# Optimization experiments

Measured on AMD Instinct MI355X. Metric: run time of the kernel, lower is better.

## Reference

```python
import jax, jax.numpy as jnp
import numpy as np

N_NODES = 50000
N_EDGES = 800000
N_FEAT = 128
HIDDEN = 64
N_CLASSES = 16


def setup_inputs() -> dict:
    key = jax.random.key(0)
    ks = jax.random.split(key, 8)
    x = jax.random.normal(ks[0], (N_NODES, N_FEAT), dtype=jnp.float32)
    edge_index = jax.random.randint(ks[1], (2, N_EDGES), 0, N_NODES, dtype=jnp.int64)
    # GCNConv weights (glorot-like) and biases
    W1 = jax.random.normal(ks[2], (N_FEAT, HIDDEN), dtype=jnp.float32) / np.sqrt(N_FEAT)
    b1 = jnp.zeros((HIDDEN,), dtype=jnp.float32)
    W2 = jax.random.normal(ks[3], (HIDDEN, HIDDEN), dtype=jnp.float32) / np.sqrt(HIDDEN)
    b2 = jnp.zeros((HIDDEN,), dtype=jnp.float32)
    Wout = jax.random.normal(ks[4], (HIDDEN, N_CLASSES), dtype=jnp.float32) / np.sqrt(HIDDEN)
    bout = jnp.zeros((N_CLASSES,), dtype=jnp.float32)
    return {"x": x, "edge_index": edge_index, "W1": W1, "b1": b1,
            "W2": W2, "b2": b2, "Wout": Wout, "bout": bout}


def _gcn_conv(h, src, dst, norm, W, b, n_nodes):
    # h: [N, F_in]; linear transform then normalized scatter-add aggregation
    h = h @ W                                   # [N, F_out]
    msg = h[src] * norm[:, None]                # gather + scale  [E+N, F_out]
    out = jax.ops.segment_sum(msg, dst, num_segments=n_nodes)  # scatter-add
    return out + b


def reference(x, edge_index, W1, b1, W2, b2, Wout, bout):
    n = x.shape[0]
    # add self-loops (PyG GCNConv default add_self_loops=True)
    loops = jnp.arange(n, dtype=edge_index.dtype)
    src = jnp.concatenate([edge_index[0], loops])
    dst = jnp.concatenate([edge_index[1], loops])
    # symmetric normalization: deg^-1/2[src] * deg^-1/2[dst] (edge_weight = 1)
    ones = jnp.ones(src.shape[0], dtype=x.dtype)
    deg = jax.ops.segment_sum(ones, dst, num_segments=n)
    dinv = jnp.where(deg > 0, jax.lax.rsqrt(jnp.maximum(deg, 1e-12)), 0.0)
    norm = dinv[src] * dinv[dst]

    h = _gcn_conv(x, src, dst, norm, W1, b1, n)
    h = jax.nn.relu(h)
    # dropout p=0.5 with training=False -> identity
    h = _gcn_conv(h, src, dst, norm, W2, b2, n)
    h = jax.nn.relu(h)
    logits = h @ Wout + bout
    return jax.nn.softmax(logits, axis=1)
```

## Files before the change

kernel.cpp:

```cpp
#include <hip/hip_runtime.h>
#include <hip/hip_fp16.h>

#define N_NODES 50000
#define N_EDGES 800000
#define N_FEAT 128
#define HIDDEN 64
#define N_CLASSES 16
#define NBLK_NODE 196
#define TCAP 8192

typedef _Float16 f16x8 __attribute__((ext_vector_type(8)));
typedef float f32x4 __attribute__((ext_vector_type(4)));

__global__ void k_init(int* __restrict__ tileCur) {
    int tid = threadIdx.x;
    if (tid < NBLK_NODE) tileCur[tid] = tid * TCAP;
}

__global__ __launch_bounds__(256) void k_part(const int* __restrict__ ei,
                                              int* __restrict__ tileCur,
                                              int* __restrict__ binned) {
    __shared__ int cnt[NBLK_NODE], base[NBLK_NODE], cur[NBLK_NODE];
    int tid = threadIdx.x;
    int start = blockIdx.x * 4096;
    if (tid < NBLK_NODE) cnt[tid] = 0;
    __syncthreads();
    int s[16], d[16];
#pragma unroll
    for (int u = 0; u < 4; ++u) {
        int e0 = start + u * 1024 + tid * 4;
        if (e0 + 4 <= N_EDGES) {
            int4 s4 = *(const int4*)&ei[e0];
            int4 d4 = *(const int4*)&ei[N_EDGES + e0];
            s[u * 4 + 0] = s4.x; s[u * 4 + 1] = s4.y; s[u * 4 + 2] = s4.z; s[u * 4 + 3] = s4.w;
            d[u * 4 + 0] = d4.x; d[u * 4 + 1] = d4.y; d[u * 4 + 2] = d4.z; d[u * 4 + 3] = d4.w;
#pragma unroll
            for (int q = 0; q < 4; ++q) atomicAdd(&cnt[d[u * 4 + q] >> 8], 1);
        } else {
#pragma unroll
            for (int q = 0; q < 4; ++q) {
                int e = e0 + q;
                if (e < N_EDGES) {
                    s[u * 4 + q] = ei[e];
                    d[u * 4 + q] = ei[N_EDGES + e];
                    atomicAdd(&cnt[d[u * 4 + q] >> 8], 1);
                } else s[u * 4 + q] = -1;
            }
        }
    }
    __syncthreads();
    if (tid < NBLK_NODE) {
        base[tid] = atomicAdd(&tileCur[tid], cnt[tid]);
        cur[tid] = 0;
    }
    __syncthreads();
#pragma unroll
    for (int u = 0; u < 16; ++u) {
        if (s[u] < 0) continue;
        int t = d[u] >> 8;
        int r = atomicAdd(&cur[t], 1);
        int p = base[t] + r;
        if (p < (t + 1) * TCAP)
            binned[p] = s[u] | ((d[u] & 255) << 16);
    }
}

__global__ __launch_bounds__(256) void k_finesort(const int* __restrict__ binned,
                                                  const int* __restrict__ tileCur,
                                                  int* __restrict__ csr,
                                                  int2* __restrict__ rse,
                                                  float* __restrict__ dinv) {
    __shared__ int stage[TCAP];
    __shared__ int sc[256];
    __shared__ int cnt256[256];
    __shared__ int nodeOff[256];
    int tid = threadIdx.x;
    int tb = blockIdx.x;
    int beg = tb * TCAP;
    int m = tileCur[tb] - beg;
    if (m > TCAP) m = TCAP;
    cnt256[tid] = 0;
    __syncthreads();
    const int4* b4 = (const int4*)(binned + beg);
    int nv = m >> 2;
    for (int i = tid; i < nv; i += 256) {
        int4 r = b4[i];
        atomicAdd(&cnt256[(r.x >> 16) & 255], 1);
        atomicAdd(&cnt256[(r.y >> 16) & 255], 1);
        atomicAdd(&cnt256[(r.z >> 16) & 255], 1);
        atomicAdd(&cnt256[(r.w >> 16) & 255], 1);
    }
    for (int i = (m & ~3) + tid; i < m; i += 256)
        atomicAdd(&cnt256[(binned[beg + i] >> 16) & 255], 1);
    __syncthreads();
    int myc = cnt256[tid];
    sc[tid] = myc;
    __syncthreads();
#pragma unroll
    for (int off = 1; off < 256; off <<= 1) {
        int t = (tid >= off) ? sc[tid - off] : 0;
        __syncthreads();
        sc[tid] += t;
        __syncthreads();
    }
    int off0 = sc[tid] - myc;
    nodeOff[tid] = off0;
    int gnode = tb * 256 + tid;
    if (gnode < N_NODES) {
        dinv[gnode] = rsqrtf((float)myc + 1.0f);
        rse[gnode] = make_int2(beg + off0, myc);
    }
    cnt256[tid] = 0;
    __syncthreads();
    for (int i = tid; i < nv; i += 256) {
        int4 r = b4[i];
        int rr;
        rr = atomicAdd(&cnt256[(r.x >> 16) & 255], 1); stage[nodeOff[(r.x >> 16) & 255] + rr] = r.x & 0xFFFF;
        rr = atomicAdd(&cnt256[(r.y >> 16) & 255], 1); stage[nodeOff[(r.y >> 16) & 255] + rr] = r.y & 0xFFFF;
        rr = atomicAdd(&cnt256[(r.z >> 16) & 255], 1); stage[nodeOff[(r.z >> 16) & 255] + rr] = r.z & 0xFFFF;
        rr = atomicAdd(&cnt256[(r.w >> 16) & 255], 1); stage[nodeOff[(r.w >> 16) & 255] + rr] = r.w & 0xFFFF;
    }
    for (int i = (m & ~3) + tid; i < m; i += 256) {
        int rec = binned[beg + i];
        int dl = (rec >> 16) & 255;
        int rr = atomicAdd(&cnt256[dl], 1);
        stage[nodeOff[dl] + rr] = rec & 0xFFFF;
    }
    __syncthreads();
    int4* c4 = (int4*)(csr + beg);
    for (int i = tid; i < nv; i += 256) c4[i] = ((const int4*)stage)[i];
    for (int i = (m & ~3) + tid; i < m; i += 256) csr[beg + i] = stage[i];
}

template <int K, typename TIn>
__global__ __launch_bounds__(256) void k_mm(const TIn* __restrict__ a,
                                            const float* __restrict__ w,
                                            const float* __restrict__ dinv,
                                            __half* __restrict__ out) {
    constexpr int LDK = K + 8;
    __shared__ __align__(16) __half A_lds[64 * LDK];
    __shared__ __align__(16) __half Wt_lds[64 * LDK];
    int tid = threadIdx.x;
    long nbase = (long)blockIdx.x * 64;

    for (int i = tid; i < K * 16; i += 256) {
        int k = (i * 4) >> 6;
        int f0 = (i * 4) & 63;
        float4 v = *(const float4*)&w[i * 4];
        Wt_lds[(f0 + 0) * LDK + k] = __float2half(v.x);
        Wt_lds[(f0 + 1) * LDK + k] = __float2half(v.y);
        Wt_lds[(f0 + 2) * LDK + k] = __float2half(v.z);
        Wt_lds[(f0 + 3) * LDK + k] = __float2half(v.w);
    }
    for (int i = tid; i < 64 * K / 8; i += 256) {
        int n = (i * 8) / K;
        int k0 = (i * 8) % K;
        long gn = nbase + n;
        if constexpr (sizeof(TIn) == 4) {
            float4 v0, v1;
            if (gn < N_NODES) {
                v0 = *(const float4*)&a[gn * K + k0];
                v1 = *(const float4*)&a[gn * K + k0 + 4];
            } else {
                v0 = make_float4(0.f, 0.f, 0.f, 0.f);
                v1 = v0;
            }
            __half2* dst = (__half2*)&A_lds[n * LDK + k0];
            dst[0] = __floats2half2_rn(v0.x, v0.y);
            dst[1] = __floats2half2_rn(v0.z, v0.w);
            dst[2] = __floats2half2_rn(v1.x, v1.y);
            dst[3] = __floats2half2_rn(v1.z, v1.w);
        } else {
            int4 v = (gn < N_NODES) ? *(const int4*)&a[gn * K + k0]
                                    : make_int4(0, 0, 0, 0);
            *(int4*)&A_lds[n * LDK + k0] = v;
        }
    }
    __syncthreads();

    int wv = tid >> 6;
    int lane = tid & 63;
    int m = lane & 15;
    int quad = lane >> 4;
    const __half* Arow = &A_lds[(wv * 16 + m) * LDK + quad * 8];
    f32x4 acc[4] = {};
#pragma unroll
    for (int t = 0; t < K; t += 32) {
        f16x8 af = *(const f16x8*)(const void*)&Arow[t];
#pragma unroll
        for (int g = 0; g < 4; ++g) {
            f16x8 bf = *(const f16x8*)(const void*)&Wt_lds[(g * 16 + m) * LDK + t + quad * 8];
            acc[g] = __builtin_amdgcn_mfma_f32_16x16x32_f16(af, bf, acc[g], 0, 0, 0);
        }
    }

#pragma unroll
    for (int r = 0; r < 4; ++r) {
        int n = wv * 16 + quad * 4 + r;
        long gn = nbase + n;
        if (gn < N_NODES) {
            float di = dinv[gn];
#pragma unroll
            for (int g = 0; g < 4; ++g)
                out[gn * HIDDEN + g * 16 + m] = __float2half(acc[g][r] * di);
        }
    }
}

__device__ __forceinline__ void acc_row8(float* a, int4 rv) {
    float2 f;
    f = __half22float2(*(__half2*)&rv.x); a[0] += f.x; a[1] += f.y;
    f = __half22float2(*(__half2*)&rv.y); a[2] += f.x; a[3] += f.y;
    f = __half22float2(*(__half2*)&rv.z); a[4] += f.x; a[5] += f.y;
    f = __half22float2(*(__half2*)&rv.w); a[6] += f.x; a[7] += f.y;
}

__global__ void k_gather(const __half* __restrict__ h, const int* __restrict__ csr,
                         const int2* __restrict__ rse, const float* __restrict__ dinv,
                         const float* __restrict__ bias, __half* __restrict__ out) {
    int t = blockIdx.x * 256 + threadIdx.x;
    int node = __builtin_amdgcn_readfirstlane(t >> 6);
    int lane = t & 63;
    int e8 = lane >> 3;
    int q = lane & 7;
    int2 se = rse[node];
    int r0 = se.x, r1 = se.x + se.y;
    float dd = dinv[node];

    float a[8] = {0.f, 0.f, 0.f, 0.f, 0.f, 0.f, 0.f, 0.f};
    if (e8 == 0)
        acc_row8(a, *(const int4*)&h[(long)node * HIDDEN + q * 8]);

    int j = r0;
    while (j + 16 <= r1) {
        int sA = csr[j + e8];
        int sB = csr[j + 8 + e8];
        int4 rA = *(const int4*)&h[(long)sA * HIDDEN + q * 8];
        int4 rB = *(const int4*)&h[(long)sB * HIDDEN + q * 8];
        acc_row8(a, rA);
        acc_row8(a, rB);
        j += 16;
    }
    if (j + 8 <= r1) {
        int sA = csr[j + e8];
        acc_row8(a, *(const int4*)&h[(long)sA * HIDDEN + q * 8]);
        j += 8;
    }
    int rem = r1 - j;
    if (e8 < rem) {
        int sA = csr[j + e8];
        acc_row8(a, *(const int4*)&h[(long)sA * HIDDEN + q * 8]);
    }
#pragma unroll
    for (int off = 8; off < 64; off <<= 1)
#pragma unroll
        for (int i = 0; i < 8; ++i) a[i] += __shfl_xor(a[i], off, 64);

    if (e8 == 0) {
        float4 b0 = *(const float4*)&bias[q * 8];
        float4 b1 = *(const float4*)&bias[q * 8 + 4];
        float r[8];
        r[0] = fmaxf(fmaf(a[0], dd, b0.x), 0.f);
        r[1] = fmaxf(fmaf(a[1], dd, b0.y), 0.f);
        r[2] = fmaxf(fmaf(a[2], dd, b0.z), 0.f);
        r[3] = fmaxf(fmaf(a[3], dd, b0.w), 0.f);
        r[4] = fmaxf(fmaf(a[4], dd, b1.x), 0.f);
        r[5] = fmaxf(fmaf(a[5], dd, b1.y), 0.f);
        r[6] = fmaxf(fmaf(a[6], dd, b1.z), 0.f);
        r[7] = fmaxf(fmaf(a[7], dd, b1.w), 0.f);
        __half2 h0 = __floats2half2_rn(r[0], r[1]);
        __half2 h1 = __floats2half2_rn(r[2], r[3]);
        __half2 h2 = __floats2half2_rn(r[4], r[5]);
        __half2 h3 = __floats2half2_rn(r[6], r[7]);
        int4 o;
        o.x = *(int*)&h0; o.y = *(int*)&h1; o.z = *(int*)&h2; o.w = *(int*)&h3;
        *(int4*)&out[(long)node * HIDDEN + q * 8] = o;
    }
}

__global__ void k_out(const __half* __restrict__ h, const float* __restrict__ w,
                      const float* __restrict__ b, float* __restrict__ out) {
    __shared__ float Ws[HIDDEN * N_CLASSES];
    __shared__ float bs[N_CLASSES];
    int tid = threadIdx.x;
    for (int i = tid; i < HIDDEN * N_CLASSES; i += 256) Ws[i] = w[i];
    if (tid < N_CLASSES) bs[tid] = b[tid];
    __syncthreads();
    int node = blockIdx.x * 16 + (tid >> 4);
    int c = tid & 15;
    const __half* hr = h + (long)node * HIDDEN;
    float acc = bs[c];
#pragma unroll
    for (int k = 0; k < HIDDEN; ++k)
        acc = fmaf(__half2float(hr[k]), Ws[k * N_CLASSES + c], acc);
    float m = acc;
#pragma unroll
    for (int off = 8; off; off >>= 1) m = fmaxf(m, __shfl_xor(m, off, 16));
    float ex = expf(acc - m);
    float s = ex;
#pragma unroll
    for (int off = 8; off; off >>= 1) s += __shfl_xor(s, off, 16);
    out[(long)node * N_CLASSES + c] = ex / s;
}

extern "C" void kernel_launch(void* const* d_in, const int* in_sizes, int n_in,
                              void* d_out, int out_size, void* d_ws, size_t ws_size,
                              hipStream_t stream) {
    const float* x    = (const float*)d_in[0];
    const int*   ei   = (const int*)d_in[1];
    const float* W1   = (const float*)d_in[2];
    const float* b1   = (const float*)d_in[3];
    const float* W2   = (const float*)d_in[4];
    const float* b2   = (const float*)d_in[5];
    const float* Wout = (const float*)d_in[6];
    const float* bout = (const float*)d_in[7];
    float* out = (float*)d_out;

    char* ws = (char*)d_ws;
    int2*   rse     = (int2*)ws;                       ws += 400128;
    float*  dinv    = (float*)ws;                      ws += 200192;
    int*    tileCur = (int*)ws;                        ws += 1024;
    int*    csr     = (int*)ws;                        ws += (size_t)NBLK_NODE * TCAP * 4;
    char*   slotA   = ws;                              ws += 6553600;
    __half* bufB    = (__half*)ws;
    int*    binned  = (int*)slotA;
    __half* bufA    = (__half*)slotA;

    const int NB_MM = (N_NODES + 63) / 64;
    const int NB_E16 = (N_EDGES + 4095) / 4096;

    k_init<<<1, 256, 0, stream>>>(tileCur);
    k_part<<<NB_E16, 256, 0, stream>>>(ei, tileCur, binned);
    k_finesort<<<NBLK_NODE, 256, 0, stream>>>(binned, tileCur, csr, rse, dinv);

    k_mm<N_FEAT, float><<<NB_MM, 256, 0, stream>>>(x, W1, dinv, bufA);
    k_gather<<<N_NODES / 4, 256, 0, stream>>>(bufA, csr, rse, dinv, b1, bufB);

    k_mm<HIDDEN, __half><<<NB_MM, 256, 0, stream>>>(bufB, W2, dinv, bufA);
    k_gather<<<N_NODES / 4, 256, 0, stream>>>(bufA, csr, rse, dinv, b2, bufB);

    k_out<<<N_NODES / 16, 256, 0, stream>>>(bufB, Wout, bout, out);
}
```

Baseline: 171.5 us.

## Fuse all GCN stages into one persistent cooperative kernel with grid syncs

Replaces the eight separate kernel launches (init, partition, finesort, two matmuls, two gathers, output softmax) with a single cooperative persistent kernel. Blocks loop over work items in each phase and are separated by grid.sync() barriers, all sharing one static shared-memory buffer. The partition phase now handles 1024-edge chunks instead of 4096, and the grid is sized from the occupancy query assuming 256 CUs. This removes per-launch overhead and inter-kernel gaps, at the cost of grid-wide barrier latency, occupancy limited by the largest shared-memory use, and more global tileCur atomics from the smaller chunks.

```diff
diff --git a/kernel.cpp b/kernel.cpp
--- a/kernel.cpp
+++ b/kernel.cpp
@@ -1,211 +1,21 @@
 #include <hip/hip_runtime.h>
 #include <hip/hip_fp16.h>
+#include <hip/hip_cooperative_groups.h>
+
+namespace cg = cooperative_groups;
 
 #define N_NODES 50000
 #define N_EDGES 800000
 #define N_FEAT 128
 #define HIDDEN 64
 #define N_CLASSES 16
-#define NBLK_NODE 196
+#define NT 196
 #define TCAP 8192
+#define NCHUNK 782
+#define SMEM_BYTES 35840
 
 typedef _Float16 f16x8 __attribute__((ext_vector_type(8)));
 typedef float f32x4 __attribute__((ext_vector_type(4)));
-
-__global__ void k_init(int* __restrict__ tileCur) {
-    int tid = threadIdx.x;
-    if (tid < NBLK_NODE) tileCur[tid] = tid * TCAP;
-}
-
-__global__ __launch_bounds__(256) void k_part(const int* __restrict__ ei,
-                                              int* __restrict__ tileCur,
-                                              int* __restrict__ binned) {
-    __shared__ int cnt[NBLK_NODE], base[NBLK_NODE], cur[NBLK_NODE];
-    int tid = threadIdx.x;
-    int start = blockIdx.x * 4096;
-    if (tid < NBLK_NODE) cnt[tid] = 0;
-    __syncthreads();
-    int s[16], d[16];
-#pragma unroll
-    for (int u = 0; u < 4; ++u) {
-        int e0 = start + u * 1024 + tid * 4;
-        if (e0 + 4 <= N_EDGES) {
-            int4 s4 = *(const int4*)&ei[e0];
-            int4 d4 = *(const int4*)&ei[N_EDGES + e0];
-            s[u * 4 + 0] = s4.x; s[u * 4 + 1] = s4.y; s[u * 4 + 2] = s4.z; s[u * 4 + 3] = s4.w;
-            d[u * 4 + 0] = d4.x; d[u * 4 + 1] = d4.y; d[u * 4 + 2] = d4.z; d[u * 4 + 3] = d4.w;
-#pragma unroll
-            for (int q = 0; q < 4; ++q) atomicAdd(&cnt[d[u * 4 + q] >> 8], 1);
-        } else {
-#pragma unroll
-            for (int q = 0; q < 4; ++q) {
-                int e = e0 + q;
-                if (e < N_EDGES) {
-                    s[u * 4 + q] = ei[e];
-                    d[u * 4 + q] = ei[N_EDGES + e];
-                    atomicAdd(&cnt[d[u * 4 + q] >> 8], 1);
-                } else s[u * 4 + q] = -1;
-            }
-        }
-    }
-    __syncthreads();
-    if (tid < NBLK_NODE) {
-        base[tid] = atomicAdd(&tileCur[tid], cnt[tid]);
-        cur[tid] = 0;
-    }
-    __syncthreads();
-#pragma unroll
-    for (int u = 0; u < 16; ++u) {
-        if (s[u] < 0) continue;
-        int t = d[u] >> 8;
-        int r = atomicAdd(&cur[t], 1);
-        int p = base[t] + r;
-        if (p < (t + 1) * TCAP)
-            binned[p] = s[u] | ((d[u] & 255) << 16);
-    }
-}
-
-__global__ __launch_bounds__(256) void k_finesort(const int* __restrict__ binned,
-                                                  const int* __restrict__ tileCur,
-                                                  int* __restrict__ csr,
-                                                  int2* __restrict__ rse,
-                                                  float* __restrict__ dinv) {
-    __shared__ int stage[TCAP];
-    __shared__ int sc[256];
-    __shared__ int cnt256[256];
-    __shared__ int nodeOff[256];
-    int tid = threadIdx.x;
-    int tb = blockIdx.x;
-    int beg = tb * TCAP;
-    int m = tileCur[tb] - beg;
-    if (m > TCAP) m = TCAP;
-    cnt256[tid] = 0;
-    __syncthreads();
-    const int4* b4 = (const int4*)(binned + beg);
-    int nv = m >> 2;
-    for (int i = tid; i < nv; i += 256) {
-        int4 r = b4[i];
-        atomicAdd(&cnt256[(r.x >> 16) & 255], 1);
-        atomicAdd(&cnt256[(r.y >> 16) & 255], 1);
-        atomicAdd(&cnt256[(r.z >> 16) & 255], 1);
-        atomicAdd(&cnt256[(r.w >> 16) & 255], 1);
-    }
-    for (int i = (m & ~3) + tid; i < m; i += 256)
-        atomicAdd(&cnt256[(binned[beg + i] >> 16) & 255], 1);
-    __syncthreads();
-    int myc = cnt256[tid];
-    sc[tid] = myc;
-    __syncthreads();
-#pragma unroll
-    for (int off = 1; off < 256; off <<= 1) {
-        int t = (tid >= off) ? sc[tid - off] : 0;
-        __syncthreads();
-        sc[tid] += t;
-        __syncthreads();
-    }
-    int off0 = sc[tid] - myc;
-    nodeOff[tid] = off0;
-    int gnode = tb * 256 + tid;
-    if (gnode < N_NODES) {
-        dinv[gnode] = rsqrtf((float)myc + 1.0f);
-        rse[gnode] = make_int2(beg + off0, myc);
-    }
-    cnt256[tid] = 0;
-    __syncthreads();
-    for (int i = tid; i < nv; i += 256) {
-        int4 r = b4[i];
-        int rr;
-        rr = atomicAdd(&cnt256[(r.x >> 16) & 255], 1); stage[nodeOff[(r.x >> 16) & 255] + rr] = r.x & 0xFFFF;
-        rr = atomicAdd(&cnt256[(r.y >> 16) & 255], 1); stage[nodeOff[(r.y >> 16) & 255] + rr] = r.y & 0xFFFF;
-        rr = atomicAdd(&cnt256[(r.z >> 16) & 255], 1); stage[nodeOff[(r.z >> 16) & 255] + rr] = r.z & 0xFFFF;
-        rr = atomicAdd(&cnt256[(r.w >> 16) & 255], 1); stage[nodeOff[(r.w >> 16) & 255] + rr] = r.w & 0xFFFF;
-    }
-    for (int i = (m & ~3) + tid; i < m; i += 256) {
-        int rec = binned[beg + i];
-        int dl = (rec >> 16) & 255;
-        int rr = atomicAdd(&cnt256[dl], 1);
-        stage[nodeOff[dl] + rr] = rec & 0xFFFF;
-    }
-    __syncthreads();
-    int4* c4 = (int4*)(csr + beg);
-    for (int i = tid; i < nv; i += 256) c4[i] = ((const int4*)stage)[i];
-    for (int i = (m & ~3) + tid; i < m; i += 256) csr[beg + i] = stage[i];
-}
-
-template <int K, typename TIn>
-__global__ __launch_bounds__(256) void k_mm(const TIn* __restrict__ a,
-                                            const float* __restrict__ w,
-                                            const float* __restrict__ dinv,
-                                            __half* __restrict__ out) {
-    constexpr int LDK = K + 8;
-    __shared__ __align__(16) __half A_lds[64 * LDK];
-    __shared__ __align__(16) __half Wt_lds[64 * LDK];
-    int tid = threadIdx.x;
-    long nbase = (long)blockIdx.x * 64;
-
-    for (int i = tid; i < K * 16; i += 256) {
-        int k = (i * 4) >> 6;
-        int f0 = (i * 4) & 63;
-        float4 v = *(const float4*)&w[i * 4];
-        Wt_lds[(f0 + 0) * LDK + k] = __float2half(v.x);
-        Wt_lds[(f0 + 1) * LDK + k] = __float2half(v.y);
-        Wt_lds[(f0 + 2) * LDK + k] = __float2half(v.z);
-        Wt_lds[(f0 + 3) * LDK + k] = __float2half(v.w);
-    }
-    for (int i = tid; i < 64 * K / 8; i += 256) {
-        int n = (i * 8) / K;
-        int k0 = (i * 8) % K;
-        long gn = nbase + n;
-        if constexpr (sizeof(TIn) == 4) {
-            float4 v0, v1;
-            if (gn < N_NODES) {
-                v0 = *(const float4*)&a[gn * K + k0];
-                v1 = *(const float4*)&a[gn * K + k0 + 4];
-            } else {
-                v0 = make_float4(0.f, 0.f, 0.f, 0.f);
-                v1 = v0;
-            }
-            __half2* dst = (__half2*)&A_lds[n * LDK + k0];
-            dst[0] = __floats2half2_rn(v0.x, v0.y);
-            dst[1] = __floats2half2_rn(v0.z, v0.w);
-            dst[2] = __floats2half2_rn(v1.x, v1.y);
-            dst[3] = __floats2half2_rn(v1.z, v1.w);
-        } else {
-            int4 v = (gn < N_NODES) ? *(const int4*)&a[gn * K + k0]
-                                    : make_int4(0, 0, 0, 0);
-            *(int4*)&A_lds[n * LDK + k0] = v;
-        }
-    }
-    __syncthreads();
-
-    int wv = tid >> 6;
-    int lane = tid & 63;
-    int m = lane & 15;
-    int quad = lane >> 4;
-    const __half* Arow = &A_lds[(wv * 16 + m) * LDK + quad * 8];
-    f32x4 acc[4] = {};
-#pragma unroll
-    for (int t = 0; t < K; t += 32) {
-        f16x8 af = *(const f16x8*)(const void*)&Arow[t];
-#pragma unroll
-        for (int g = 0; g < 4; ++g) {
-            f16x8 bf = *(const f16x8*)(const void*)&Wt_lds[(g * 16 + m) * LDK + t + quad * 8];
-            acc[g] = __builtin_amdgcn_mfma_f32_16x16x32_f16(af, bf, acc[g], 0, 0, 0);
-        }
-    }
-
-#pragma unroll
-    for (int r = 0; r < 4; ++r) {
-        int n = wv * 16 + quad * 4 + r;
-        long gn = nbase + n;
-        if (gn < N_NODES) {
-            float di = dinv[gn];
-#pragma unroll
-            for (int g = 0; g < 4; ++g)
-                out[gn * HIDDEN + g * 16 + m] = __float2half(acc[g][r] * di);
-        }
-    }
-}
 
 __device__ __forceinline__ void acc_row8(float* a, int4 rv) {
     float2 f;
@@ -215,22 +25,19 @@
     f = __half22float2(*(__half2*)&rv.w); a[6] += f.x; a[7] += f.y;
 }
 
-__global__ void k_gather(const __half* __restrict__ h, const int* __restrict__ csr,
-                         const int2* __restrict__ rse, const float* __restrict__ dinv,
-                         const float* __restrict__ bias, __half* __restrict__ out) {
-    int t = blockIdx.x * 256 + threadIdx.x;
-    int node = __builtin_amdgcn_readfirstlane(t >> 6);
-    int lane = t & 63;
-    int e8 = lane >> 3;
-    int q = lane & 7;
+__device__ __forceinline__ void gather_node(const __half* __restrict__ h,
+                                            const int* __restrict__ csr,
+                                            const int2* __restrict__ rse,
+                                            const float* __restrict__ dinv,
+                                            const float* __restrict__ bias,
+                                            __half* __restrict__ out,
+                                            int node, int e8, int q) {
     int2 se = rse[node];
     int r0 = se.x, r1 = se.x + se.y;
     float dd = dinv[node];
-
     float a[8] = {0.f, 0.f, 0.f, 0.f, 0.f, 0.f, 0.f, 0.f};
     if (e8 == 0)
         acc_row8(a, *(const int4*)&h[(long)node * HIDDEN + q * 8]);
-
     int j = r0;
     while (j + 16 <= r1) {
         int sA = csr[j + e8];
@@ -278,29 +85,266 @@
     }
 }
 
-__global__ void k_out(const __half* __restrict__ h, const float* __restrict__ w,
-                      const float* __restrict__ b, float* __restrict__ out) {
-    __shared__ float Ws[HIDDEN * N_CLASSES];
-    __shared__ float bs[N_CLASSES];
+template <int K, typename TIn>
+__device__ __forceinline__ void mm_phase(const TIn* __restrict__ a,
+                                         const float* __restrict__ w,
+                                         const float* __restrict__ dinv,
+                                         __half* __restrict__ out,
+                                         int bid, int nB, char* smem) {
+    constexpr int LDK = K + 8;
+    __half* A_lds = (__half*)smem;
+    __half* Wt_lds = (__half*)(smem + 64 * LDK * 2);
     int tid = threadIdx.x;
-    for (int i = tid; i < HIDDEN * N_CLASSES; i += 256) Ws[i] = w[i];
-    if (tid < N_CLASSES) bs[tid] = b[tid];
-    __syncthreads();
-    int node = blockIdx.x * 16 + (tid >> 4);
-    int c = tid & 15;
-    const __half* hr = h + (long)node * HIDDEN;
-    float acc = bs[c];
-#pragma unroll
-    for (int k = 0; k < HIDDEN; ++k)
-        acc = fmaf(__half2float(hr[k]), Ws[k * N_CLASSES + c], acc);
-    float m = acc;
-#pragma unroll
-    for (int off = 8; off; off >>= 1) m = fmaxf(m, __shfl_xor(m, off, 16));
-    float ex = expf(acc - m);
-    float s = ex;
-#pragma unroll
-    for (int off = 8; off; off >>= 1) s += __shfl_xor(s, off, 16);
-    out[(long)node * N_CLASSES + c] = ex / s;
+    for (int i = tid; i < K * 16; i += 256) {
+        int k = (i * 4) >> 6;
+        int f0 = (i * 4) & 63;
+        float4 v = *(const float4*)&w[i * 4];
+        Wt_lds[(f0 + 0) * LDK + k] = __float2half(v.x);
+        Wt_lds[(f0 + 1) * LDK + k] = __float2half(v.y);
+        Wt_lds[(f0 + 2) * LDK + k] = __float2half(v.z);
+        Wt_lds[(f0 + 3) * LDK + k] = __float2half(v.w);
+    }
+    int wv = tid >> 6;
+    int lane = tid & 63;
+    int mr = lane & 15;
+    int quad = lane >> 4;
+    for (int tile = bid; tile < (N_NODES + 63) / 64; tile += nB) {
+        __syncthreads();
+        long nbase = (long)tile * 64;
+        for (int i = tid; i < 64 * K / 8; i += 256) {
+            int n = (i * 8) / K;
+            int k0 = (i * 8) % K;
+            long gn = nbase + n;
+            if constexpr (sizeof(TIn) == 4) {
+                float4 v0, v1;
+                if (gn < N_NODES) {
+                    v0 = *(const float4*)&a[gn * K + k0];
+                    v1 = *(const float4*)&a[gn * K + k0 + 4];
+                } else {
+                    v0 = make_float4(0.f, 0.f, 0.f, 0.f);
+                    v1 = v0;
+                }
+                __half2* dst = (__half2*)&A_lds[n * LDK + k0];
+                dst[0] = __floats2half2_rn(v0.x, v0.y);
+                dst[1] = __floats2half2_rn(v0.z, v0.w);
+                dst[2] = __floats2half2_rn(v1.x, v1.y);
+                dst[3] = __floats2half2_rn(v1.z, v1.w);
+            } else {
+                int4 v = (gn < N_NODES) ? *(const int4*)&a[gn * K + k0]
+                                        : make_int4(0, 0, 0, 0);
+                *(int4*)&A_lds[n * LDK + k0] = v;
+            }
+        }
+        __syncthreads();
+        const __half* Arow = &A_lds[(wv * 16 + mr) * LDK + quad * 8];
+        f32x4 acc[4] = {};
+#pragma unroll
+        for (int t = 0; t < K; t += 32) {
+            f16x8 af = *(const f16x8*)(const void*)&Arow[t];
+#pragma unroll
+            for (int g = 0; g < 4; ++g) {
+                f16x8 bf = *(const f16x8*)(const void*)&Wt_lds[(g * 16 + mr) * LDK + t + quad * 8];
+                acc[g] = __builtin_amdgcn_mfma_f32_16x16x32_f16(af, bf, acc[g], 0, 0, 0);
+            }
+        }
+#pragma unroll
+        for (int r = 0; r < 4; ++r) {
+            int n = wv * 16 + quad * 4 + r;
+            long gn = nbase + n;
+            if (gn < N_NODES) {
+                float di = dinv[gn];
+#pragma unroll
+                for (int g = 0; g < 4; ++g)
+                    out[gn * HIDDEN + g * 16 + mr] = __float2half(acc[g][r] * di);
+            }
+        }
+    }
+}
+
+__global__ __launch_bounds__(256, 4) void mega(
+    const float* __restrict__ x, const int* __restrict__ ei,
+    const float* __restrict__ W1, const float* __restrict__ b1,
+    const float* __restrict__ W2, const float* __restrict__ b2,
+    const float* __restrict__ Wout, const float* __restrict__ bout,
+    float* __restrict__ out,
+    int* __restrict__ tileCur, int* __restrict__ binned, int* __restrict__ csr,
+    int2* __restrict__ rse, float* __restrict__ dinv,
+    __half* __restrict__ bufA, __half* __restrict__ bufB) {
+    cg::grid_group grid = cg::this_grid();
+    __shared__ __align__(16) char smem[SMEM_BYTES];
+    int tid = threadIdx.x;
+    int bid = blockIdx.x;
+    int nB = gridDim.x;
+
+    for (int i = bid * 256 + tid; i < NT; i += nB * 256) tileCur[i] = i * TCAP;
+    grid.sync();
+
+    {
+        int* cnt = (int*)smem;
+        int* base = cnt + NT;
+        int* cur = base + NT;
+        for (int cb = bid; cb < NCHUNK; cb += nB) {
+            if (tid < NT) cnt[tid] = 0;
+            __syncthreads();
+            int s[4], d[4];
+            int e0 = cb * 1024 + tid * 4;
+            if (e0 + 4 <= N_EDGES) {
+                int4 s4 = *(const int4*)&ei[e0];
+                int4 d4 = *(const int4*)&ei[N_EDGES + e0];
+                s[0] = s4.x; s[1] = s4.y; s[2] = s4.z; s[3] = s4.w;
+                d[0] = d4.x; d[1] = d4.y; d[2] = d4.z; d[3] = d4.w;
+#pragma unroll
+                for (int u = 0; u < 4; ++u) atomicAdd(&cnt[d[u] >> 8], 1);
+            } else {
+#pragma unroll
+                for (int u = 0; u < 4; ++u) {
+                    int e = e0 + u;
+                    if (e < N_EDGES) {
+                        s[u] = ei[e];
+                        d[u] = ei[N_EDGES + e];
+                        atomicAdd(&cnt[d[u] >> 8], 1);
+                    } else s[u] = -1;
+                }
+            }
+            __syncthreads();
+            if (tid < NT) {
+                base[tid] = atomicAdd(&tileCur[tid], cnt[tid]);
+                cur[tid] = 0;
+            }
+            __syncthreads();
+#pragma unroll
+            for (int u = 0; u < 4; ++u) {
+                if (s[u] < 0) continue;
+                int t = d[u] >> 8;
+                int r = atomicAdd(&cur[t], 1);
+                int p = base[t] + r;
+                if (p >= t * TCAP && p < (t + 1) * TCAP)
+                    binned[p] = s[u] | ((d[u] & 255) << 16);
+            }
+            __syncthreads();
+        }
+    }
+    grid.sync();
+
+    {
+        int* stage = (int*)smem;
+        int* cnt256 = (int*)(smem + TCAP * 4);
+        int* sc = cnt256 + 256;
+        int* nodeOff = sc + 256;
+        for (int tb = bid; tb < NT; tb += nB) {
+            int beg = tb * TCAP;
+            int m = tileCur[tb] - beg;
+            if (m > TCAP) m = TCAP;
+            if (m < 0) m = 0;
+            cnt256[tid] = 0;
+            __syncthreads();
+            const int4* b4 = (const int4*)(binned + beg);
+            int nv = m >> 2;
+            for (int i = tid; i < nv; i += 256) {
+                int4 r = b4[i];
+                atomicAdd(&cnt256[(r.x >> 16) & 255], 1);
+                atomicAdd(&cnt256[(r.y >> 16) & 255], 1);
+                atomicAdd(&cnt256[(r.z >> 16) & 255], 1);
+                atomicAdd(&cnt256[(r.w >> 16) & 255], 1);
+            }
+            for (int i = (m & ~3) + tid; i < m; i += 256)
+                atomicAdd(&cnt256[(binned[beg + i] >> 16) & 255], 1);
+            __syncthreads();
+            int myc = cnt256[tid];
+            sc[tid] = myc;
+            __syncthreads();
+#pragma unroll
+            for (int off = 1; off < 256; off <<= 1) {
+                int t = (tid >= off) ? sc[tid - off] : 0;
+                __syncthreads();
+                sc[tid] += t;
+                __syncthreads();
+            }
+            int off0 = sc[tid] - myc;
+            nodeOff[tid] = off0;
+            int gnode = tb * 256 + tid;
+            if (gnode < N_NODES) {
+                dinv[gnode] = rsqrtf((float)myc + 1.0f);
+                rse[gnode] = make_int2(beg + off0, myc);
+            }
+            cnt256[tid] = 0;
+            __syncthreads();
+            for (int i = tid; i < nv; i += 256) {
+                int4 r = b4[i];
+                int rr;
+                rr = atomicAdd(&cnt256[(r.x >> 16) & 255], 1); stage[nodeOff[(r.x >> 16) & 255] + rr] = r.x & 0xFFFF;
+                rr = atomicAdd(&cnt256[(r.y >> 16) & 255], 1); stage[nodeOff[(r.y >> 16) & 255] + rr] = r.y & 0xFFFF;
+                rr = atomicAdd(&cnt256[(r.z >> 16) & 255], 1); stage[nodeOff[(r.z >> 16) & 255] + rr] = r.z & 0xFFFF;
+                rr = atomicAdd(&cnt256[(r.w >> 16) & 255], 1); stage[nodeOff[(r.w >> 16) & 255] + rr] = r.w & 0xFFFF;
+            }
+            for (int i = (m & ~3) + tid; i < m; i += 256) {
+                int rec = binned[beg + i];
+                int dl = (rec >> 16) & 255;
+                int rr = atomicAdd(&cnt256[dl], 1);
+                stage[nodeOff[dl] + rr] = rec & 0xFFFF;
+            }
+            __syncthreads();
+            int4* c4 = (int4*)(csr + beg);
+            for (int i = tid; i < nv; i += 256) c4[i] = ((const int4*)stage)[i];
+            for (int i = (m & ~3) + tid; i < m; i += 256) csr[beg + i] = stage[i];
+            __syncthreads();
+        }
+    }
+    grid.sync();
+
+    mm_phase<N_FEAT, float>(x, W1, dinv, bufA, bid, nB, smem);
+    grid.sync();
+
+    {
+        int wv = tid >> 6;
+        int lane = tid & 63;
+        int e8 = lane >> 3, q = lane & 7;
+        for (int vb = bid; vb < N_NODES / 4; vb += nB) {
+            int node = __builtin_amdgcn_readfirstlane(vb * 4 + wv);
+            gather_node(bufA, csr, rse, dinv, b1, bufB, node, e8, q);
+        }
+    }
+    grid.sync();
+
+    mm_phase<HIDDEN, __half>(bufB, W2, dinv, bufA, bid, nB, smem);
+    grid.sync();
+
+    {
+        int wv = tid >> 6;
+        int lane = tid & 63;
+        int e8 = lane >> 3, q = lane & 7;
+        for (int vb = bid; vb < N_NODES / 4; vb += nB) {
+            int node = __builtin_amdgcn_readfirstlane(vb * 4 + wv);
+            gather_node(bufA, csr, rse, dinv, b2, bufB, node, e8, q);
+        }
+    }
+    grid.sync();
+
+    {
+        float* Ws = (float*)smem;
+        float* bs = Ws + HIDDEN * N_CLASSES;
+        for (int i = tid; i < HIDDEN * N_CLASSES; i += 256) Ws[i] = Wout[i];
+        if (tid < N_CLASSES) bs[tid] = bout[tid];
+        __syncthreads();
+        int c = tid & 15;
+        int sub = tid >> 4;
+        for (int g = bid; g < N_NODES / 16; g += nB) {
+            int node = g * 16 + sub;
+            const __half* hr = bufB + (long)node * HIDDEN;
+            float acc = bs[c];
+#pragma unroll
+            for (int k = 0; k < HIDDEN; ++k)
+                acc = fmaf(__half2float(hr[k]), Ws[k * N_CLASSES + c], acc);
+            float m2 = acc;
+#pragma unroll
+            for (int off = 8; off; off >>= 1) m2 = fmaxf(m2, __shfl_xor(m2, off, 16));
+            float ex = expf(acc - m2);
+            float s = ex;
+#pragma unroll
+            for (int off = 8; off; off >>= 1) s += __shfl_xor(s, off, 16);
+            out[(long)node * N_CLASSES + c] = ex / s;
+        }
+    }
 }
 
 extern "C" void kernel_launch(void* const* d_in, const int* in_sizes, int n_in,
@@ -320,24 +364,22 @@
     int2*   rse     = (int2*)ws;                       ws += 400128;
     float*  dinv    = (float*)ws;                      ws += 200192;
     int*    tileCur = (int*)ws;                        ws += 1024;
-    int*    csr     = (int*)ws;                        ws += (size_t)NBLK_NODE * TCAP * 4;
+    int*    csr     = (int*)ws;                        ws += (size_t)NT * TCAP * 4;
     char*   slotA   = ws;                              ws += 6553600;
     __half* bufB    = (__half*)ws;
     int*    binned  = (int*)slotA;
     __half* bufA    = (__half*)slotA;
 
-    const int NB_MM = (N_NODES + 63) / 64;
-    const int NB_E16 = (N_EDGES + 4095) / 4096;
-
-    k_init<<<1, 256, 0, stream>>>(tileCur);
-    k_part<<<NB_E16, 256, 0, stream>>>(ei, tileCur, binned);
-    k_finesort<<<NBLK_NODE, 256, 0, stream>>>(binned, tileCur, csr, rse, dinv);
-
-    k_mm<N_FEAT, float><<<NB_MM, 256, 0, stream>>>(x, W1, dinv, bufA);
-    k_gather<<<N_NODES / 4, 256, 0, stream>>>(bufA, csr, rse, dinv, b1, bufB);
-
-    k_mm<HIDDEN, __half><<<NB_MM, 256, 0, stream>>>(bufB, W2, dinv, bufA);
-    k_gather<<<N_NODES / 4, 256, 0, stream>>>(bufA, csr, rse, dinv, b2, bufB);
-
-    k_out<<<N_NODES / 16, 256, 0, stream>>>(bufB, Wout, bout, out);
-}
+    int maxb = 0;
+    if (hipOccupancyMaxActiveBlocksPerMultiprocessor(&maxb, mega, 256, 0) != hipSuccess || maxb < 1)
+        maxb = 2;
+    if (maxb > 8) maxb = 8;
+    int G = maxb * 256;
+
+    void* kargs[] = {
+        (void*)&x, (void*)&ei, (void*)&W1, (void*)&b1, (void*)&W2, (void*)&b2,
+        (void*)&Wout, (void*)&bout, (void*)&out,
+        (void*)&tileCur, (void*)&binned, (void*)&csr,
+        (void*)&rse, (void*)&dinv, (void*)&bufA, (void*)&bufB};
+    hipLaunchCooperativeKernel(mega, dim3(G), dim3(256), kargs, 0, stream);
+}
```

New measurement: 640.7 us. 274% more time.
